# Performance work log

Measured on AMD Instinct MI355X. Metric: run time of the kernel, lower is better.

The kernel has to match this reference:

```python
import jax, jax.numpy as jnp
import numpy as np

D = 1024
S = 4096

def setup_inputs() -> dict:
    key = jax.random.key(0)
    ks = jax.random.split(key, 7)
    x = jax.random.normal(ks[0], (S, D), dtype=jnp.float32)
    scale = 1.0 / np.sqrt(D)
    wq = jax.random.normal(ks[1], (D, D), dtype=jnp.float32) * scale
    wk = jax.random.normal(ks[2], (D, D), dtype=jnp.float32) * scale
    wv = jax.random.normal(ks[3], (D, D), dtype=jnp.float32) * scale
    bq = jax.random.normal(ks[4], (D,), dtype=jnp.float32) * 0.01
    bk = jax.random.normal(ks[5], (D,), dtype=jnp.float32) * 0.01
    bv = jax.random.normal(ks[6], (D,), dtype=jnp.float32) * 0.01
    return {"x": x, "wq": wq, "bq": bq, "wk": wk, "bk": bk, "wv": wv, "bv": bv}

def reference(x, wq, bq, wk, bk, wv, bv):
    # q = x @ wq^T + bq  (torch nn.Linear convention: weight [out,in])
    q = x @ wq.T + bq            # [S, D]
    k = x @ wk.T + bk            # [S, D]
    v = x @ wv.T + bv            # [S, D]
    inv_sqrt_d = 1.0 / jnp.sqrt(jnp.asarray(x.shape[1], dtype=x.dtype))
    scores = (q @ k.T) * inv_sqrt_d      # [S, S]
    attn = jax.nn.softmax(scores, axis=-1)
    return attn @ v                      # [S, D]
```

## Files before the change

kernel.cpp:

```cpp
#include <hip/hip_runtime.h>
#include <stdint.h>
#include <stddef.h>

#define SEQ 4096
#define DIM 1024

typedef __bf16 bf16x8 __attribute__((ext_vector_type(8)));
typedef float floatx4 __attribute__((ext_vector_type(4)));
typedef unsigned short u16x8 __attribute__((ext_vector_type(8)));

__device__ __forceinline__ unsigned short f2b(float f) {
  union { float f; unsigned u; } v; v.f = f;
  unsigned u = v.u;
  unsigned r = (u + 0x7FFFu + ((u >> 16) & 1u)) >> 16;
  return (unsigned short)r;
}
__device__ __forceinline__ float b2f(unsigned short h) {
  union { unsigned u; float f; } v; v.u = ((unsigned)h) << 16;
  return v.f;
}

__global__ void cvt_f32_bf16(const float* __restrict__ in,
                             unsigned short* __restrict__ out, int n) {
  int i = (blockIdx.x * blockDim.x + threadIdx.x) * 4;
  if (i < n) {
    float4 f = *(const float4*)(in + i);
    ushort4 o;
    o.x = f2b(f.x); o.y = f2b(f.y); o.z = f2b(f.z); o.w = f2b(f.w);
    *(ushort4*)(out + i) = o;
  }
}

__device__ __forceinline__ void gemm_core(
    const unsigned short* __restrict__ A,
    const unsigned short* __restrict__ B,
    int lda, int ldb, int kext,
    unsigned short* As, unsigned short* Bs,
    floatx4 acc[4][4]) {
  const int tid  = threadIdx.x;
  const int lane = tid & 63;
  const int wave = tid >> 6;
  const int sub_m = (wave >> 1) * 64;
  const int sub_n = (wave & 1) * 64;
  const int col  = lane & 15;
  const int quad = lane >> 4;

  const int srow  = tid >> 3;
  const int sgran = (tid & 7) ^ (srow & 7);
  const int scol  = sgran * 8;
  const int dflat = tid * 8;

  const unsigned short* Ag = A + (size_t)srow * lda + scol;
  const unsigned short* Bg = B + (size_t)srow * ldb + scol;

  for (int k0 = 0; k0 < kext; k0 += 64) {
    __syncthreads();
#pragma unroll
    for (int j = 0; j < 4; j++) {
      __builtin_amdgcn_global_load_lds(
          (const __attribute__((address_space(1))) void*)(Ag + (size_t)(j * 32) * lda + k0),
          (__attribute__((address_space(3))) void*)(&As[j * 2048 + dflat]), 16, 0, 0);
      __builtin_amdgcn_global_load_lds(
          (const __attribute__((address_space(1))) void*)(Bg + (size_t)(j * 32) * ldb + k0),
          (__attribute__((address_space(3))) void*)(&Bs[j * 2048 + dflat]), 16, 0, 0);
    }
    __syncthreads();
#pragma unroll
    for (int ks = 0; ks < 64; ks += 32) {
      const int gbase = ks >> 3;
      bf16x8 af[4], bfr[4];
#pragma unroll
      for (int i = 0; i < 4; i++) {
        const int R = sub_m + 16 * i + col;
        const int slot = (gbase + quad) ^ (R & 7);
        af[i] = *(const bf16x8*)&As[R * 64 + slot * 8];
      }
#pragma unroll
      for (int j = 0; j < 4; j++) {
        const int R = sub_n + 16 * j + col;
        const int slot = (gbase + quad) ^ (R & 7);
        bfr[j] = *(const bf16x8*)&Bs[R * 64 + slot * 8];
      }
#pragma unroll
      for (int i = 0; i < 4; i++)
#pragma unroll
        for (int j = 0; j < 4; j++)
          acc[i][j] = __builtin_amdgcn_mfma_f32_16x16x32_bf16(af[i], bfr[j],
                                                              acc[i][j], 0, 0, 0);
    }
  }
}


__global__ __launch_bounds__(256, 2)
void qkv_gemm(const unsigned short* __restrict__ xb,
              const unsigned short* __restrict__ wqb,
              const unsigned short* __restrict__ wkb,
              const unsigned short* __restrict__ wvb,
              const float* __restrict__ bq, const float* __restrict__ bk,
              const float* __restrict__ bv,
              unsigned short* __restrict__ qb, unsigned short* __restrict__ kb,
              unsigned short* __restrict__ vtb) {
  __shared__ unsigned short As[8192];
  __shared__ unsigned short Bs[8192];
  const int z = blockIdx.z;
  const unsigned short* W = (z == 0) ? wqb : (z == 1) ? wkb : wvb;
  const float* bias = (z == 0) ? bq : (z == 1) ? bk : bv;
  const int tile_m = blockIdx.y * 128;
  const int tile_n = blockIdx.x * 128;

  floatx4 acc[4][4];
#pragma unroll
  for (int i = 0; i < 4; i++)
#pragma unroll
    for (int j = 0; j < 4; j++) acc[i][j] = (floatx4)0.0f;

  gemm_core(xb + (size_t)tile_m * DIM, W + (size_t)tile_n * DIM,
            DIM, DIM, DIM, As, Bs, acc);

  const int lane = threadIdx.x & 63;
  const int wave = threadIdx.x >> 6;
  const int sub_m = (wave >> 1) * 64;
  const int sub_n = (wave & 1) * 64;
  const int col  = lane & 15;
  const int quad = lane >> 4;

  float biasv[4];
#pragma unroll
  for (int j = 0; j < 4; j++) biasv[j] = bias[tile_n + sub_n + 16 * j + col];

  unsigned short* outp = (z == 0) ? qb : kb;
#pragma unroll
  for (int i = 0; i < 4; i++) {
#pragma unroll
    for (int j = 0; j < 4; j++) {
#pragma unroll
      for (int r = 0; r < 4; r++) {
        const int m = tile_m + sub_m + 16 * i + quad * 4 + r;
        const int n = tile_n + sub_n + 16 * j + col;
        const unsigned short v = f2b(acc[i][j][r] + biasv[j]);
        if (z < 2)
          outp[(size_t)m * DIM + n] = v;
        else
          vtb[(size_t)n * SEQ + m] = v;
      }
    }
  }
}

__global__ __launch_bounds__(256, 2)
void score_gemm(const unsigned short* __restrict__ qb,
                const unsigned short* __restrict__ kb,
                unsigned short* __restrict__ sc, float scale) {
  __shared__ unsigned short As[8192];
  __shared__ unsigned short Bs[8192];
  const int tile_m = blockIdx.y * 128;
  const int tile_n = blockIdx.x * 128;

  floatx4 acc[4][4];
#pragma unroll
  for (int i = 0; i < 4; i++)
#pragma unroll
    for (int j = 0; j < 4; j++) acc[i][j] = (floatx4)0.0f;

  gemm_core(qb + (size_t)tile_m * DIM, kb + (size_t)tile_n * DIM,
            DIM, DIM, DIM, As, Bs, acc);

  const int lane = threadIdx.x & 63;
  const int wave = threadIdx.x >> 6;
  const int sub_m = (wave >> 1) * 64;
  const int sub_n = (wave & 1) * 64;
  const int col  = lane & 15;
  const int quad = lane >> 4;
#pragma unroll
  for (int i = 0; i < 4; i++) {
#pragma unroll
    for (int j = 0; j < 4; j++) {
#pragma unroll
      for (int r = 0; r < 4; r++) {
        const int m = tile_m + sub_m + 16 * i + quad * 4 + r;
        const int n = tile_n + sub_n + 16 * j + col;
        sc[(size_t)m * SEQ + n] = f2b(acc[i][j][r] * scale);
      }
    }
  }
}

__global__ __launch_bounds__(256, 2)
void pv_gemm(const unsigned short* __restrict__ sc,
             const unsigned short* __restrict__ vtb,
             float* __restrict__ out0, float* __restrict__ out1) {
  __shared__ unsigned short As[8192];
  __shared__ unsigned short Bs[8192];
  const int z = blockIdx.z;
  const int koff = z * (SEQ / 2);
  float* C = z ? out1 : out0;
  const int tile_m = blockIdx.y * 128;
  const int tile_n = blockIdx.x * 128;

  floatx4 acc[4][4];
#pragma unroll
  for (int i = 0; i < 4; i++)
#pragma unroll
    for (int j = 0; j < 4; j++) acc[i][j] = (floatx4)0.0f;

  gemm_core(sc + (size_t)tile_m * SEQ + koff,
            vtb + (size_t)tile_n * SEQ + koff,
            SEQ, SEQ, SEQ / 2, As, Bs, acc);

  const int lane = threadIdx.x & 63;
  const int wave = threadIdx.x >> 6;
  const int sub_m = (wave >> 1) * 64;
  const int sub_n = (wave & 1) * 64;
  const int col  = lane & 15;
  const int quad = lane >> 4;
#pragma unroll
  for (int i = 0; i < 4; i++) {
#pragma unroll
    for (int j = 0; j < 4; j++) {
#pragma unroll
      for (int r = 0; r < 4; r++) {
        const int m = tile_m + sub_m + 16 * i + quad * 4 + r;
        const int n = tile_n + sub_n + 16 * j + col;
        C[(size_t)m * DIM + n] = acc[i][j][r];
      }
    }
  }
}

__global__ __launch_bounds__(256)
void reduce_add(float* __restrict__ out, const float* __restrict__ part) {
  const int i = (blockIdx.x * 256 + threadIdx.x) * 4;
  float4 a = *(const float4*)(out + i);
  float4 b = *(const float4*)(part + i);
  a.x += b.x; a.y += b.y; a.z += b.z; a.w += b.w;
  *(float4*)(out + i) = a;
}

__global__ __launch_bounds__(256)
void softmax_inplace(unsigned short* __restrict__ P) {
  const int row = blockIdx.x;
  unsigned short* p = P + (size_t)row * SEQ;
  const int tid  = threadIdx.x;
  const int lane = tid & 63;
  const int wave = tid >> 6;

  u16x8 raw0 = *(const u16x8*)(p + tid * 16);
  u16x8 raw1 = *(const u16x8*)(p + tid * 16 + 8);
  float v[16];
#pragma unroll
  for (int k = 0; k < 8; k++) v[k] = b2f(raw0[k]);
#pragma unroll
  for (int k = 0; k < 8; k++) v[8 + k] = b2f(raw1[k]);

  float mx = -1e30f;
#pragma unroll
  for (int k = 0; k < 16; k++) mx = fmaxf(mx, v[k]);
#pragma unroll
  for (int off = 32; off > 0; off >>= 1) mx = fmaxf(mx, __shfl_xor(mx, off, 64));
  __shared__ float redm[4];
  __shared__ float reds[4];
  if (lane == 0) redm[wave] = mx;
  __syncthreads();
  mx = fmaxf(fmaxf(redm[0], redm[1]), fmaxf(redm[2], redm[3]));

  float sum = 0.0f;
#pragma unroll
  for (int k = 0; k < 16; k++) {
    v[k] = exp2f((v[k] - mx) * 1.44269504f);
    sum += v[k];
  }
#pragma unroll
  for (int off = 32; off > 0; off >>= 1) sum += __shfl_xor(sum, off, 64);
  if (lane == 0) reds[wave] = sum;
  __syncthreads();
  sum = reds[0] + reds[1] + reds[2] + reds[3];
  const float inv = 1.0f / sum;

  u16x8 o0, o1;
#pragma unroll
  for (int k = 0; k < 8; k++) o0[k] = f2b(v[k] * inv);
#pragma unroll
  for (int k = 0; k < 8; k++) o1[k] = f2b(v[8 + k] * inv);
  *(u16x8*)(p + tid * 16) = o0;
  *(u16x8*)(p + tid * 16 + 8) = o1;
}

extern "C" void kernel_launch(void* const* d_in, const int* in_sizes, int n_in,
                              void* d_out, int out_size, void* d_ws, size_t ws_size,
                              hipStream_t stream) {
  const float* x  = (const float*)d_in[0];
  const float* wq = (const float*)d_in[1];
  const float* bq = (const float*)d_in[2];
  const float* wk = (const float*)d_in[3];
  const float* bk = (const float*)d_in[4];
  const float* wv = (const float*)d_in[5];
  const float* bv = (const float*)d_in[6];

  uint8_t* ws = (uint8_t*)d_ws;
  unsigned short* xb  = (unsigned short*)(ws);
  unsigned short* wqb = (unsigned short*)(ws + ((size_t)8  << 20));
  unsigned short* wkb = (unsigned short*)(ws + ((size_t)10 << 20));
  unsigned short* wvb = (unsigned short*)(ws + ((size_t)12 << 20));
  unsigned short* qb  = (unsigned short*)(ws + ((size_t)14 << 20));
  unsigned short* kb  = (unsigned short*)(ws + ((size_t)22 << 20));
  unsigned short* vtb = (unsigned short*)(ws + ((size_t)30 << 20));
  unsigned short* sc  = (unsigned short*)(ws + ((size_t)38 << 20));
  float*          part = (float*)(ws);

  cvt_f32_bf16<<<(SEQ * DIM) / 1024, 256, 0, stream>>>(x, xb, SEQ * DIM);
  cvt_f32_bf16<<<(DIM * DIM) / 1024, 256, 0, stream>>>(wq, wqb, DIM * DIM);
  cvt_f32_bf16<<<(DIM * DIM) / 1024, 256, 0, stream>>>(wk, wkb, DIM * DIM);
  cvt_f32_bf16<<<(DIM * DIM) / 1024, 256, 0, stream>>>(wv, wvb, DIM * DIM);

  qkv_gemm<<<dim3(DIM / 128, SEQ / 128, 3), 256, 0, stream>>>(
      xb, wqb, wkb, wvb, bq, bk, bv, qb, kb, vtb);

  score_gemm<<<dim3(SEQ / 128, SEQ / 128), 256, 0, stream>>>(qb, kb, sc, 0.03125f);

  softmax_inplace<<<SEQ, 256, 0, stream>>>(sc);

  pv_gemm<<<dim3(DIM / 128, SEQ / 128, 2), 256, 0, stream>>>(
      sc, vtb, (float*)d_out, part);

  reduce_add<<<(SEQ * DIM) / 1024, 256, 0, stream>>>((float*)d_out, part);
}
```

Before: 220.5 us.

## Use 32x32 MFMA tiles, grouped tile swizzle, and fuse input conversions

Switches the shared GEMM core from 16x16x32 to 32x32x16 bf16 MFMA, so each wave computes its 64x64 sub-tile as a 2x2 grid of 16-wide accumulators with fewer LDS fragment reads per FLOP. Adds a grouped block-index swizzle to all three GEMMs to improve L2 reuse of A/B tiles across neighbouring blocks. Merges the four fp32-to-bf16 conversion launches into one kernel to cut launch overhead. The new epilogue index mapping must match the 32x32 MFMA output layout, and stores become strided across more rows per lane.

After: 225.7 us. 2.4% more time.

```diff
diff --git a/kernel.cpp b/kernel.cpp
--- a/kernel.cpp
+++ b/kernel.cpp
@@ -7,6 +7,7 @@
 
 typedef __bf16 bf16x8 __attribute__((ext_vector_type(8)));
 typedef float floatx4 __attribute__((ext_vector_type(4)));
+typedef float floatx16 __attribute__((ext_vector_type(16)));
 typedef unsigned short u16x8 __attribute__((ext_vector_type(8)));
 
 __device__ __forceinline__ unsigned short f2b(float f) {
@@ -20,15 +21,34 @@
   return v.f;
 }
 
-__global__ void cvt_f32_bf16(const float* __restrict__ in,
-                             unsigned short* __restrict__ out, int n) {
-  int i = (blockIdx.x * blockDim.x + threadIdx.x) * 4;
-  if (i < n) {
-    float4 f = *(const float4*)(in + i);
-    ushort4 o;
-    o.x = f2b(f.x); o.y = f2b(f.y); o.z = f2b(f.z); o.w = f2b(f.w);
-    *(ushort4*)(out + i) = o;
-  }
+__global__ __launch_bounds__(256)
+void cvt_all(const float* __restrict__ x, const float* __restrict__ wq,
+             const float* __restrict__ wk, const float* __restrict__ wv,
+             unsigned short* __restrict__ xb, unsigned short* __restrict__ wqb,
+             unsigned short* __restrict__ wkb, unsigned short* __restrict__ wvb) {
+  const int bid = blockIdx.x;
+  const float* src;
+  unsigned short* dst;
+  int off;
+  if (bid < 4096)      { src = x;  dst = xb;  off = bid; }
+  else if (bid < 5120) { src = wq; dst = wqb; off = bid - 4096; }
+  else if (bid < 6144) { src = wk; dst = wkb; off = bid - 5120; }
+  else                 { src = wv; dst = wvb; off = bid - 6144; }
+  const int i = off * 1024 + threadIdx.x * 4;
+  float4 f = *(const float4*)(src + i);
+  ushort4 o;
+  o.x = f2b(f.x); o.y = f2b(f.y); o.z = f2b(f.z); o.w = f2b(f.w);
+  *(ushort4*)(dst + i) = o;
+}
+
+__device__ __forceinline__ void swizzle_tiles(int gx, int gy, int& bx, int& by) {
+  const int pid = blockIdx.y * gx + blockIdx.x;
+  const int GM = 8;
+  const int group = pid / (GM * gx);
+  const int first = group * GM;
+  const int gsz = (gy - first) < GM ? (gy - first) : GM;
+  by = first + (pid % gsz);
+  bx = (pid % (GM * gx)) / gsz;
 }
 
 __device__ __forceinline__ void gemm_core(
@@ -36,14 +56,14 @@
     const unsigned short* __restrict__ B,
     int lda, int ldb, int kext,
     unsigned short* As, unsigned short* Bs,
-    floatx4 acc[4][4]) {
+    floatx16 acc[2][2]) {
   const int tid  = threadIdx.x;
   const int lane = tid & 63;
   const int wave = tid >> 6;
   const int sub_m = (wave >> 1) * 64;
   const int sub_n = (wave & 1) * 64;
-  const int col  = lane & 15;
-  const int quad = lane >> 4;
+  const int r31   = lane & 31;
+  const int khalf = lane >> 5;
 
   const int srow  = tid >> 3;
   const int sgran = (tid & 7) ^ (srow & 7);
@@ -66,26 +86,24 @@
     }
     __syncthreads();
 #pragma unroll
-    for (int ks = 0; ks < 64; ks += 32) {
-      const int gbase = ks >> 3;
-      bf16x8 af[4], bfr[4];
-#pragma unroll
-      for (int i = 0; i < 4; i++) {
-        const int R = sub_m + 16 * i + col;
-        const int slot = (gbase + quad) ^ (R & 7);
-        af[i] = *(const bf16x8*)&As[R * 64 + slot * 8];
-      }
-#pragma unroll
-      for (int j = 0; j < 4; j++) {
-        const int R = sub_n + 16 * j + col;
-        const int slot = (gbase + quad) ^ (R & 7);
-        bfr[j] = *(const bf16x8*)&Bs[R * 64 + slot * 8];
-      }
-#pragma unroll
-      for (int i = 0; i < 4; i++)
-#pragma unroll
-        for (int j = 0; j < 4; j++)
-          acc[i][j] = __builtin_amdgcn_mfma_f32_16x16x32_bf16(af[i], bfr[j],
+    for (int ks = 0; ks < 64; ks += 16) {
+      const int g = (ks >> 3) + khalf;
+      bf16x8 af[2], bfr[2];
+#pragma unroll
+      for (int i = 0; i < 2; i++) {
+        const int R = sub_m + 32 * i + r31;
+        af[i] = *(const bf16x8*)&As[R * 64 + (g ^ (R & 7)) * 8];
+      }
+#pragma unroll
+      for (int j = 0; j < 2; j++) {
+        const int R = sub_n + 32 * j + r31;
+        bfr[j] = *(const bf16x8*)&Bs[R * 64 + (g ^ (R & 7)) * 8];
+      }
+#pragma unroll
+      for (int i = 0; i < 2; i++)
+#pragma unroll
+        for (int j = 0; j < 2; j++)
+          acc[i][j] = __builtin_amdgcn_mfma_f32_32x32x16_bf16(af[i], bfr[j],
                                                               acc[i][j], 0, 0, 0);
     }
   }
@@ -106,14 +124,16 @@
   const int z = blockIdx.z;
   const unsigned short* W = (z == 0) ? wqb : (z == 1) ? wkb : wvb;
   const float* bias = (z == 0) ? bq : (z == 1) ? bk : bv;
-  const int tile_m = blockIdx.y * 128;
-  const int tile_n = blockIdx.x * 128;
-
-  floatx4 acc[4][4];
-#pragma unroll
-  for (int i = 0; i < 4; i++)
-#pragma unroll
-    for (int j = 0; j < 4; j++) acc[i][j] = (floatx4)0.0f;
+  int bx, by;
+  swizzle_tiles(gridDim.x, gridDim.y, bx, by);
+  const int tile_m = by * 128;
+  const int tile_n = bx * 128;
+
+  floatx16 acc[2][2];
+#pragma unroll
+  for (int i = 0; i < 2; i++)
+#pragma unroll
+    for (int j = 0; j < 2; j++) acc[i][j] = (floatx16)0.0f;
 
   gemm_core(xb + (size_t)tile_m * DIM, W + (size_t)tile_n * DIM,
             DIM, DIM, DIM, As, Bs, acc);
@@ -122,22 +142,22 @@
   const int wave = threadIdx.x >> 6;
   const int sub_m = (wave >> 1) * 64;
   const int sub_n = (wave & 1) * 64;
-  const int col  = lane & 15;
-  const int quad = lane >> 4;
-
-  float biasv[4];
-#pragma unroll
-  for (int j = 0; j < 4; j++) biasv[j] = bias[tile_n + sub_n + 16 * j + col];
+  const int r31 = lane & 31;
+  const int rowoff = 4 * (lane >> 5);
+
+  float biasv[2];
+#pragma unroll
+  for (int j = 0; j < 2; j++) biasv[j] = bias[tile_n + sub_n + 32 * j + r31];
 
   unsigned short* outp = (z == 0) ? qb : kb;
 #pragma unroll
-  for (int i = 0; i < 4; i++) {
-#pragma unroll
-    for (int j = 0; j < 4; j++) {
-#pragma unroll
-      for (int r = 0; r < 4; r++) {
-        const int m = tile_m + sub_m + 16 * i + quad * 4 + r;
-        const int n = tile_n + sub_n + 16 * j + col;
+  for (int i = 0; i < 2; i++) {
+#pragma unroll
+    for (int j = 0; j < 2; j++) {
+#pragma unroll
+      for (int r = 0; r < 16; r++) {
+        const int m = tile_m + sub_m + 32 * i + (r & 3) + 8 * (r >> 2) + rowoff;
+        const int n = tile_n + sub_n + 32 * j + r31;
         const unsigned short v = f2b(acc[i][j][r] + biasv[j]);
         if (z < 2)
           outp[(size_t)m * DIM + n] = v;
@@ -154,14 +174,16 @@
                 unsigned short* __restrict__ sc, float scale) {
   __shared__ unsigned short As[8192];
   __shared__ unsigned short Bs[8192];
-  const int tile_m = blockIdx.y * 128;
-  const int tile_n = blockIdx.x * 128;
-
-  floatx4 acc[4][4];
-#pragma unroll
-  for (int i = 0; i < 4; i++)
-#pragma unroll
-    for (int j = 0; j < 4; j++) acc[i][j] = (floatx4)0.0f;
+  int bx, by;
+  swizzle_tiles(gridDim.x, gridDim.y, bx, by);
+  const int tile_m = by * 128;
+  const int tile_n = bx * 128;
+
+  floatx16 acc[2][2];
+#pragma unroll
+  for (int i = 0; i < 2; i++)
+#pragma unroll
+    for (int j = 0; j < 2; j++) acc[i][j] = (floatx16)0.0f;
 
   gemm_core(qb + (size_t)tile_m * DIM, kb + (size_t)tile_n * DIM,
             DIM, DIM, DIM, As, Bs, acc);
@@ -170,16 +192,16 @@
   const int wave = threadIdx.x >> 6;
   const int sub_m = (wave >> 1) * 64;
   const int sub_n = (wave & 1) * 64;
-  const int col  = lane & 15;
-  const int quad = lane >> 4;
-#pragma unroll
-  for (int i = 0; i < 4; i++) {
-#pragma unroll
-    for (int j = 0; j < 4; j++) {
-#pragma unroll
-      for (int r = 0; r < 4; r++) {
-        const int m = tile_m + sub_m + 16 * i + quad * 4 + r;
-        const int n = tile_n + sub_n + 16 * j + col;
+  const int r31 = lane & 31;
+  const int rowoff = 4 * (lane >> 5);
+#pragma unroll
+  for (int i = 0; i < 2; i++) {
+#pragma unroll
+    for (int j = 0; j < 2; j++) {
+#pragma unroll
+      for (int r = 0; r < 16; r++) {
+        const int m = tile_m + sub_m + 32 * i + (r & 3) + 8 * (r >> 2) + rowoff;
+        const int n = tile_n + sub_n + 32 * j + r31;
         sc[(size_t)m * SEQ + n] = f2b(acc[i][j][r] * scale);
       }
     }
@@ -195,14 +217,16 @@
   const int z = blockIdx.z;
   const int koff = z * (SEQ / 2);
   float* C = z ? out1 : out0;
-  const int tile_m = blockIdx.y * 128;
-  const int tile_n = blockIdx.x * 128;
-
-  floatx4 acc[4][4];
-#pragma unroll
-  for (int i = 0; i < 4; i++)
-#pragma unroll
-    for (int j = 0; j < 4; j++) acc[i][j] = (floatx4)0.0f;
+  int bx, by;
+  swizzle_tiles(gridDim.x, gridDim.y, bx, by);
+  const int tile_m = by * 128;
+  const int tile_n = bx * 128;
+
+  floatx16 acc[2][2];
+#pragma unroll
+  for (int i = 0; i < 2; i++)
+#pragma unroll
+    for (int j = 0; j < 2; j++) acc[i][j] = (floatx16)0.0f;
 
   gemm_core(sc + (size_t)tile_m * SEQ + koff,
             vtb + (size_t)tile_n * SEQ + koff,
@@ -212,16 +236,16 @@
   const int wave = threadIdx.x >> 6;
   const int sub_m = (wave >> 1) * 64;
   const int sub_n = (wave & 1) * 64;
-  const int col  = lane & 15;
-  const int quad = lane >> 4;
-#pragma unroll
-  for (int i = 0; i < 4; i++) {
-#pragma unroll
-    for (int j = 0; j < 4; j++) {
-#pragma unroll
-      for (int r = 0; r < 4; r++) {
-        const int m = tile_m + sub_m + 16 * i + quad * 4 + r;
-        const int n = tile_n + sub_n + 16 * j + col;
+  const int r31 = lane & 31;
+  const int rowoff = 4 * (lane >> 5);
+#pragma unroll
+  for (int i = 0; i < 2; i++) {
+#pragma unroll
+    for (int j = 0; j < 2; j++) {
+#pragma unroll
+      for (int r = 0; r < 16; r++) {
+        const int m = tile_m + sub_m + 32 * i + (r & 3) + 8 * (r >> 2) + rowoff;
+        const int n = tile_n + sub_n + 32 * j + r31;
         C[(size_t)m * DIM + n] = acc[i][j][r];
       }
     }
@@ -308,10 +332,7 @@
   unsigned short* sc  = (unsigned short*)(ws + ((size_t)38 << 20));
   float*          part = (float*)(ws);
 
-  cvt_f32_bf16<<<(SEQ * DIM) / 1024, 256, 0, stream>>>(x, xb, SEQ * DIM);
-  cvt_f32_bf16<<<(DIM * DIM) / 1024, 256, 0, stream>>>(wq, wqb, DIM * DIM);
-  cvt_f32_bf16<<<(DIM * DIM) / 1024, 256, 0, stream>>>(wk, wkb, DIM * DIM);
-  cvt_f32_bf16<<<(DIM * DIM) / 1024, 256, 0, stream>>>(wv, wvb, DIM * DIM);
+  cvt_all<<<7168, 256, 0, stream>>>(x, wq, wk, wv, xb, wqb, wkb, wvb);
 
   qkv_gemm<<<dim3(DIM / 128, SEQ / 128, 3), 256, 0, stream>>>(
       xb, wqb, wkb, wvb, bq, bk, bv, qb, kb, vtb);
```

## Fuse conversions, compute V transposed directly, swizzle tiles, drop split-K in PV

Applied to the files above, without the earlier changes.

The four f32-to-bf16 conversion launches become one kernel. The V projection is computed as Wv·x^T so its transposed output is written row-contiguous instead of as strided scatter stores. The score GEMM uses grouped tile swizzling to improve L2 reuse. The PV GEMM drops its split-K plus reduce pass in favour of 64x128 tiles over the full K, which removes the partial buffer and the extra reduction kernel. The trade-off is longer per-block K loops in PV and smaller tiles with less reuse per block.

Measured after the change: 223.8 us. No clear change (+1.5%).

```diff
diff --git a/kernel.cpp b/kernel.cpp
--- a/kernel.cpp
+++ b/kernel.cpp
@@ -20,18 +20,37 @@
   return v.f;
 }
 
-__global__ void cvt_f32_bf16(const float* __restrict__ in,
-                             unsigned short* __restrict__ out, int n) {
-  int i = (blockIdx.x * blockDim.x + threadIdx.x) * 4;
-  if (i < n) {
-    float4 f = *(const float4*)(in + i);
-    ushort4 o;
-    o.x = f2b(f.x); o.y = f2b(f.y); o.z = f2b(f.z); o.w = f2b(f.w);
-    *(ushort4*)(out + i) = o;
-  }
-}
-
-__device__ __forceinline__ void gemm_core(
+__global__ __launch_bounds__(256)
+void cvt_all(const float* __restrict__ x, const float* __restrict__ wq,
+             const float* __restrict__ wk, const float* __restrict__ wv,
+             unsigned short* __restrict__ xb, unsigned short* __restrict__ wqb,
+             unsigned short* __restrict__ wkb, unsigned short* __restrict__ wvb) {
+  const int bid = blockIdx.x;
+  const float* src;
+  unsigned short* dst;
+  int off;
+  if (bid < 4096)      { src = x;  dst = xb;  off = bid; }
+  else if (bid < 5120) { src = wq; dst = wqb; off = bid - 4096; }
+  else if (bid < 6144) { src = wk; dst = wkb; off = bid - 5120; }
+  else                 { src = wv; dst = wvb; off = bid - 6144; }
+  const int i = off * 1024 + threadIdx.x * 4;
+  float4 f = *(const float4*)(src + i);
+  ushort4 o;
+  o.x = f2b(f.x); o.y = f2b(f.y); o.z = f2b(f.z); o.w = f2b(f.w);
+  *(ushort4*)(dst + i) = o;
+}
+
+__device__ __forceinline__ void swizzle_tiles(int gx, int gy, int& bx, int& by) {
+  const int pid = blockIdx.y * gx + blockIdx.x;
+  const int GM = 8;
+  const int group = pid / (GM * gx);
+  const int first = group * GM;
+  const int gsz = (gy - first) < GM ? (gy - first) : GM;
+  by = first + (pid % gsz);
+  bx = (pid % (GM * gx)) / gsz;
+}
+
+__device__ __forceinline__ void gemm_core128(
     const unsigned short* __restrict__ A,
     const unsigned short* __restrict__ B,
     int lda, int ldb, int kext,
@@ -91,6 +110,66 @@
   }
 }
 
+__device__ __forceinline__ void gemm_core64(
+    const unsigned short* __restrict__ A,
+    const unsigned short* __restrict__ B,
+    int lda, int ldb, int kext,
+    unsigned short* As, unsigned short* Bs,
+    floatx4 acc[4][2]) {
+  const int tid  = threadIdx.x;
+  const int lane = tid & 63;
+  const int wave = tid >> 6;
+  const int sub_n = wave * 32;
+  const int col  = lane & 15;
+  const int quad = lane >> 4;
+
+  const int srow  = tid >> 3;
+  const int sgran = (tid & 7) ^ (srow & 7);
+  const int scol  = sgran * 8;
+  const int dflat = tid * 8;
+
+  const unsigned short* Ag = A + (size_t)srow * lda + scol;
+  const unsigned short* Bg = B + (size_t)srow * ldb + scol;
+
+  for (int k0 = 0; k0 < kext; k0 += 64) {
+    __syncthreads();
+#pragma unroll
+    for (int j = 0; j < 2; j++)
+      __builtin_amdgcn_global_load_lds(
+          (const __attribute__((address_space(1))) void*)(Ag + (size_t)(j * 32) * lda + k0),
+          (__attribute__((address_space(3))) void*)(&As[j * 2048 + dflat]), 16, 0, 0);
+#pragma unroll
+    for (int j = 0; j < 4; j++)
+      __builtin_amdgcn_global_load_lds(
+          (const __attribute__((address_space(1))) void*)(Bg + (size_t)(j * 32) * ldb + k0),
+          (__attribute__((address_space(3))) void*)(&Bs[j * 2048 + dflat]), 16, 0, 0);
+    __syncthreads();
+#pragma unroll
+    for (int ks = 0; ks < 64; ks += 32) {
+      const int gbase = ks >> 3;
+      bf16x8 af[4], bfr[2];
+#pragma unroll
+      for (int i = 0; i < 4; i++) {
+        const int R = 16 * i + col;
+        const int slot = (gbase + quad) ^ (R & 7);
+        af[i] = *(const bf16x8*)&As[R * 64 + slot * 8];
+      }
+#pragma unroll
+      for (int j = 0; j < 2; j++) {
+        const int R = sub_n + 16 * j + col;
+        const int slot = (gbase + quad) ^ (R & 7);
+        bfr[j] = *(const bf16x8*)&Bs[R * 64 + slot * 8];
+      }
+#pragma unroll
+      for (int i = 0; i < 4; i++)
+#pragma unroll
+        for (int j = 0; j < 2; j++)
+          acc[i][j] = __builtin_amdgcn_mfma_f32_16x16x32_bf16(af[i], bfr[j],
+                                                              acc[i][j], 0, 0, 0);
+    }
+  }
+}
+
 
 __global__ __launch_bounds__(256, 2)
 void qkv_gemm(const unsigned short* __restrict__ xb,
@@ -104,19 +183,13 @@
   __shared__ unsigned short As[8192];
   __shared__ unsigned short Bs[8192];
   const int z = blockIdx.z;
-  const unsigned short* W = (z == 0) ? wqb : (z == 1) ? wkb : wvb;
-  const float* bias = (z == 0) ? bq : (z == 1) ? bk : bv;
-  const int tile_m = blockIdx.y * 128;
-  const int tile_n = blockIdx.x * 128;
+  const int pid = blockIdx.x;
 
   floatx4 acc[4][4];
 #pragma unroll
   for (int i = 0; i < 4; i++)
 #pragma unroll
     for (int j = 0; j < 4; j++) acc[i][j] = (floatx4)0.0f;
-
-  gemm_core(xb + (size_t)tile_m * DIM, W + (size_t)tile_n * DIM,
-            DIM, DIM, DIM, As, Bs, acc);
 
   const int lane = threadIdx.x & 63;
   const int wave = threadIdx.x >> 6;
@@ -125,25 +198,50 @@
   const int col  = lane & 15;
   const int quad = lane >> 4;
 
-  float biasv[4];
-#pragma unroll
-  for (int j = 0; j < 4; j++) biasv[j] = bias[tile_n + sub_n + 16 * j + col];
-
-  unsigned short* outp = (z == 0) ? qb : kb;
-#pragma unroll
-  for (int i = 0; i < 4; i++) {
-#pragma unroll
-    for (int j = 0; j < 4; j++) {
-#pragma unroll
-      for (int r = 0; r < 4; r++) {
-        const int m = tile_m + sub_m + 16 * i + quad * 4 + r;
-        const int n = tile_n + sub_n + 16 * j + col;
-        const unsigned short v = f2b(acc[i][j][r] + biasv[j]);
-        if (z < 2)
-          outp[(size_t)m * DIM + n] = v;
-        else
-          vtb[(size_t)n * SEQ + m] = v;
-      }
+  if (z < 2) {
+    const unsigned short* W = z ? wkb : wqb;
+    const float* bias = z ? bk : bq;
+    unsigned short* outp = z ? kb : qb;
+    const int by = pid >> 3, bx = pid & 7;
+    const int tile_m = by * 128, tile_n = bx * 128;
+
+    gemm_core128(xb + (size_t)tile_m * DIM, W + (size_t)tile_n * DIM,
+                 DIM, DIM, DIM, As, Bs, acc);
+
+    float biasv[4];
+#pragma unroll
+    for (int j = 0; j < 4; j++) biasv[j] = bias[tile_n + sub_n + 16 * j + col];
+#pragma unroll
+    for (int i = 0; i < 4; i++)
+#pragma unroll
+      for (int j = 0; j < 4; j++)
+#pragma unroll
+        for (int r = 0; r < 4; r++) {
+          const int m = tile_m + sub_m + 16 * i + quad * 4 + r;
+          const int n = tile_n + sub_n + 16 * j + col;
+          outp[(size_t)m * DIM + n] = f2b(acc[i][j][r] + biasv[j]);
+        }
+  } else {
+    const int by = pid >> 5, bx = pid & 31;
+    const int tile_m = by * 128, tile_n = bx * 128;
+
+    gemm_core128(wvb + (size_t)tile_m * DIM, xb + (size_t)tile_n * DIM,
+                 DIM, DIM, DIM, As, Bs, acc);
+
+#pragma unroll
+    for (int i = 0; i < 4; i++) {
+      const float* bp = &bv[tile_m + sub_m + 16 * i + quad * 4];
+      float bm[4];
+#pragma unroll
+      for (int r = 0; r < 4; r++) bm[r] = bp[r];
+#pragma unroll
+      for (int j = 0; j < 4; j++)
+#pragma unroll
+        for (int r = 0; r < 4; r++) {
+          const int m = tile_m + sub_m + 16 * i + quad * 4 + r;
+          const int n = tile_n + sub_n + 16 * j + col;
+          vtb[(size_t)m * SEQ + n] = f2b(acc[i][j][r] + bm[r]);
+        }
     }
   }
 }
@@ -154,8 +252,10 @@
                 unsigned short* __restrict__ sc, float scale) {
   __shared__ unsigned short As[8192];
   __shared__ unsigned short Bs[8192];
-  const int tile_m = blockIdx.y * 128;
-  const int tile_n = blockIdx.x * 128;
+  int bx, by;
+  swizzle_tiles(gridDim.x, gridDim.y, bx, by);
+  const int tile_m = by * 128;
+  const int tile_n = bx * 128;
 
   floatx4 acc[4][4];
 #pragma unroll
@@ -163,8 +263,8 @@
 #pragma unroll
     for (int j = 0; j < 4; j++) acc[i][j] = (floatx4)0.0f;
 
-  gemm_core(qb + (size_t)tile_m * DIM, kb + (size_t)tile_n * DIM,
-            DIM, DIM, DIM, As, Bs, acc);
+  gemm_core128(qb + (size_t)tile_m * DIM, kb + (size_t)tile_n * DIM,
+               DIM, DIM, DIM, As, Bs, acc);
 
   const int lane = threadIdx.x & 63;
   const int wave = threadIdx.x >> 6;
@@ -173,68 +273,50 @@
   const int col  = lane & 15;
   const int quad = lane >> 4;
 #pragma unroll
-  for (int i = 0; i < 4; i++) {
-#pragma unroll
-    for (int j = 0; j < 4; j++) {
+  for (int i = 0; i < 4; i++)
+#pragma unroll
+    for (int j = 0; j < 4; j++)
 #pragma unroll
       for (int r = 0; r < 4; r++) {
         const int m = tile_m + sub_m + 16 * i + quad * 4 + r;
         const int n = tile_n + sub_n + 16 * j + col;
         sc[(size_t)m * SEQ + n] = f2b(acc[i][j][r] * scale);
       }
-    }
-  }
 }
 
 __global__ __launch_bounds__(256, 2)
 void pv_gemm(const unsigned short* __restrict__ sc,
              const unsigned short* __restrict__ vtb,
-             float* __restrict__ out0, float* __restrict__ out1) {
-  __shared__ unsigned short As[8192];
+             float* __restrict__ out) {
+  __shared__ unsigned short As[4096];
   __shared__ unsigned short Bs[8192];
-  const int z = blockIdx.z;
-  const int koff = z * (SEQ / 2);
-  float* C = z ? out1 : out0;
-  const int tile_m = blockIdx.y * 128;
+  const int tile_m = blockIdx.y * 64;
   const int tile_n = blockIdx.x * 128;
 
-  floatx4 acc[4][4];
+  floatx4 acc[4][2];
 #pragma unroll
   for (int i = 0; i < 4; i++)
 #pragma unroll
-    for (int j = 0; j < 4; j++) acc[i][j] = (floatx4)0.0f;
-
-  gemm_core(sc + (size_t)tile_m * SEQ + koff,
-            vtb + (size_t)tile_n * SEQ + koff,
-            SEQ, SEQ, SEQ / 2, As, Bs, acc);
+    for (int j = 0; j < 2; j++) acc[i][j] = (floatx4)0.0f;
+
+  gemm_core64(sc + (size_t)tile_m * SEQ, vtb + (size_t)tile_n * SEQ,
+              SEQ, SEQ, SEQ, As, Bs, acc);
 
   const int lane = threadIdx.x & 63;
   const int wave = threadIdx.x >> 6;
-  const int sub_m = (wave >> 1) * 64;
-  const int sub_n = (wave & 1) * 64;
+  const int sub_n = wave * 32;
   const int col  = lane & 15;
   const int quad = lane >> 4;
 #pragma unroll
-  for (int i = 0; i < 4; i++) {
-#pragma unroll
-    for (int j = 0; j < 4; j++) {
+  for (int i = 0; i < 4; i++)
+#pragma unroll
+    for (int j = 0; j < 2; j++)
 #pragma unroll
       for (int r = 0; r < 4; r++) {
-        const int m = tile_m + sub_m + 16 * i + quad * 4 + r;
+        const int m = tile_m + 16 * i + quad * 4 + r;
         const int n = tile_n + sub_n + 16 * j + col;
-        C[(size_t)m * DIM + n] = acc[i][j][r];
-      }
-    }
-  }
-}
-
-__global__ __launch_bounds__(256)
-void reduce_add(float* __restrict__ out, const float* __restrict__ part) {
-  const int i = (blockIdx.x * 256 + threadIdx.x) * 4;
-  float4 a = *(const float4*)(out + i);
-  float4 b = *(const float4*)(part + i);
-  a.x += b.x; a.y += b.y; a.z += b.z; a.w += b.w;
-  *(float4*)(out + i) = a;
+        out[(size_t)m * DIM + n] = acc[i][j][r];
+      }
 }
 
 __global__ __launch_bounds__(256)
@@ -306,22 +388,15 @@
   unsigned short* kb  = (unsigned short*)(ws + ((size_t)22 << 20));
   unsigned short* vtb = (unsigned short*)(ws + ((size_t)30 << 20));
   unsigned short* sc  = (unsigned short*)(ws + ((size_t)38 << 20));
-  float*          part = (float*)(ws);
-
-  cvt_f32_bf16<<<(SEQ * DIM) / 1024, 256, 0, stream>>>(x, xb, SEQ * DIM);
-  cvt_f32_bf16<<<(DIM * DIM) / 1024, 256, 0, stream>>>(wq, wqb, DIM * DIM);
-  cvt_f32_bf16<<<(DIM * DIM) / 1024, 256, 0, stream>>>(wk, wkb, DIM * DIM);
-  cvt_f32_bf16<<<(DIM * DIM) / 1024, 256, 0, stream>>>(wv, wvb, DIM * DIM);
-
-  qkv_gemm<<<dim3(DIM / 128, SEQ / 128, 3), 256, 0, stream>>>(
+
+  cvt_all<<<7168, 256, 0, stream>>>(x, wq, wk, wv, xb, wqb, wkb, wvb);
+
+  qkv_gemm<<<dim3(256, 1, 3), 256, 0, stream>>>(
       xb, wqb, wkb, wvb, bq, bk, bv, qb, kb, vtb);
 
   score_gemm<<<dim3(SEQ / 128, SEQ / 128), 256, 0, stream>>>(qb, kb, sc, 0.03125f);
 
   softmax_inplace<<<SEQ, 256, 0, stream>>>(sc);
 
-  pv_gemm<<<dim3(DIM / 128, SEQ / 128, 2), 256, 0, stream>>>(
-      sc, vtb, (float*)d_out, part);
-
-  reduce_add<<<(SEQ * DIM) / 1024, 256, 0, stream>>>((float*)d_out, part);
-}
+  pv_gemm<<<dim3(DIM / 128, SEQ / 64), 256, 0, stream>>>(sc, vtb, (float*)d_out);
+}
```
